# Optimization experiments

Hardware: AMD Instinct MI355X
Metric: run time of the kernel (lower is better)

The kernel has to match this reference:

```python
import jax, jax.numpy as jnp
import numpy as np

N = 12288      # number of nodes
D = 256        # in_features
K = 31         # k_neighbours + 1
EPS = 1e-12    # F.normalize eps


def setup_inputs() -> dict:
    key = jax.random.key(0)
    k1, k2, k3 = jax.random.split(key, 3)
    x = jax.random.normal(k1, (N, D), dtype=jnp.float32)
    # Attentive layer params: elementwise feature weights (torch init is ones;
    # perturb so the reference is non-degenerate)
    w0 = 1.0 + 0.1 * jax.random.normal(k2, (D,), dtype=jnp.float32)
    w1 = 1.0 + 0.1 * jax.random.normal(k3, (D,), dtype=jnp.float32)
    return {"x": x, "w0": w0, "w1": w1}


def reference(x, w0, w1):
    # internal_forward: relu(Attentive_0(x)) then Attentive_1 (last layer, no act)
    h = jax.nn.relu(x * w0)          # [N, D]
    h = h * w1                        # [N, D]
    # F.normalize(dim=-1, p=2)
    norm = jnp.sqrt(jnp.sum(h * h, axis=-1, keepdims=True))
    h = h / jnp.maximum(norm, EPS)
    # cal_similarity_graph: dense NxN similarity
    s = jnp.einsum('nd,md->nm', h, h)  # [N, N]
    # graph_top_K: keep top-K entries per row, zero the rest (scatter mask)
    _, idx = jax.lax.top_k(s, K)       # idx: [N, K]
    rows = jnp.arange(s.shape[0])[:, None]
    mask = jnp.zeros_like(s).at[rows, idx].set(1.0)
    # apply_non_linearity 'relu'
    return jax.nn.relu(s * mask)
```

## Files before the change

### kernel.cpp

```cpp
#include <hip/hip_runtime.h>
#include <cstdint>
#include <cstddef>
#include <math.h>

#define N_NODES 12288
#define D_FEAT  256
#define K_TOP   31

typedef float nfloat4 __attribute__((ext_vector_type(4)));

__device__ __forceinline__ float np_g(float xv, float w0v, float w1v) {
  #pragma clang fp contract(off)
  float t = __fmul_rn(xv, w0v);
  t = fmaxf(t, 0.0f);
  return __fmul_rn(t, w1v);
}

__device__ __forceinline__ void nt_store4(float* p, float4 v) {
  nfloat4 nv;
  nv.x = v.x; nv.y = v.y; nv.z = v.z; nv.w = v.w;
  __builtin_nontemporal_store(nv, reinterpret_cast<nfloat4*>(p));
}

__global__ __launch_bounds__(256) void np_norm_kernel(
    const float* __restrict__ x, const float* __restrict__ w0,
    const float* __restrict__ w1, float* __restrict__ nrm) {
  #pragma clang fp contract(off)
  const int n = blockIdx.x * blockDim.x + threadIdx.x;
  if (n >= N_NODES) return;
  const float* xr = x + (size_t)n * D_FEAT;
  float blk[2];
  #pragma unroll
  for (int b = 0; b < 2; ++b) {
    float r[8];
    #pragma unroll
    for (int j = 0; j < 8; ++j) {
      const int d = 128 * b + j;
      const float g = np_g(xr[d], w0[d], w1[d]);
      r[j] = __fmul_rn(g, g);
    }
    for (int i = 8; i < 128; i += 8) {
      #pragma unroll
      for (int j = 0; j < 8; ++j) {
        const int d = 128 * b + i + j;
        const float g = np_g(xr[d], w0[d], w1[d]);
        r[j] = __fadd_rn(r[j], __fmul_rn(g, g));
      }
    }
    blk[b] = __fadd_rn(
        __fadd_rn(__fadd_rn(r[0], r[1]), __fadd_rn(r[2], r[3])),
        __fadd_rn(__fadd_rn(r[4], r[5]), __fadd_rn(r[6], r[7])));
  }
  const float tot = __fadd_rn(blk[0], blk[1]);
  nrm[n] = fmaxf(__fsqrt_rn(tot), 1e-12f);
}

__global__ __launch_bounds__(256) void np_h_kernel(
    const float* __restrict__ x, const float* __restrict__ w0,
    const float* __restrict__ w1, const float* __restrict__ nrm,
    float* __restrict__ h) {
  #pragma clang fp contract(off)
  const int q = blockIdx.x * blockDim.x + threadIdx.x;
  const int base = q * 4;
  if (base >= N_NODES * D_FEAT) return;
  const int n = base >> 8;
  const int d = base & (D_FEAT - 1);
  const float ia = nrm[n];
  const float4 xv = *reinterpret_cast<const float4*>(&x[base]);
  const float4 w0v = *reinterpret_cast<const float4*>(&w0[d]);
  const float4 w1v = *reinterpret_cast<const float4*>(&w1[d]);
  float4 o;
  o.x = __fdiv_rn(np_g(xv.x, w0v.x, w1v.x), ia);
  o.y = __fdiv_rn(np_g(xv.y, w0v.y, w1v.y), ia);
  o.z = __fdiv_rn(np_g(xv.z, w0v.z, w1v.z), ia);
  o.w = __fdiv_rn(np_g(xv.w, w0v.w, w1v.w), ia);
  *reinterpret_cast<float4*>(&h[base]) = o;
}

#define BT 128
#define BK 32
#define TBW 132
#define NTILES (N_NODES / BT)
#define NBLOCKS (NTILES * (NTILES + 1) / 2)

template <int PRE>
__global__ __launch_bounds__(256, 4) void np_gemm_kernel(
    const float* __restrict__ x, const float* __restrict__ w0,
    const float* __restrict__ w1, const float* __restrict__ nrm,
    const float* __restrict__ h, float* __restrict__ out) {
  #pragma clang fp contract(off)
  __shared__ __align__(16) float smem[2 * BK * BT];
  float (*As)[BT] = reinterpret_cast<float (*)[BT]>(smem);
  float (*Bs)[BT] = reinterpret_cast<float (*)[BT]>(smem + BK * BT);
  float (*tb)[TBW] = reinterpret_cast<float (*)[TBW]>(smem);

  const int L = blockIdx.x;
  int by = (int)(96.5 - sqrt(96.5 * 96.5 - 2.0 * (double)L));
  while (by > 0 && by * NTILES - by * (by - 1) / 2 > L) --by;
  while ((by + 1) * NTILES - (by + 1) * by / 2 <= L) ++by;
  const int bx = by + (L - (by * NTILES - by * (by - 1) / 2));

  const int n0 = by * BT;
  const int m0 = bx * BT;
  const int t = threadIdx.x;
  const int tx = t & 15, ty = t >> 4;
  const int sr = t >> 1;
  const int sk = (t & 1) * 16;

  float acc[8][8] = {};

  for (int k0 = 0; k0 < D_FEAT; k0 += BK) {
    __syncthreads();
    if (PRE) {
      #pragma unroll
      for (int q = 0; q < 4; ++q) {
        const int c = sk + q * 4;
        const float4 ha = *reinterpret_cast<const float4*>(
            &h[(size_t)(n0 + sr) * D_FEAT + k0 + c]);
        const float4 hb = *reinterpret_cast<const float4*>(
            &h[(size_t)(m0 + sr) * D_FEAT + k0 + c]);
        As[c + 0][sr] = ha.x; As[c + 1][sr] = ha.y;
        As[c + 2][sr] = ha.z; As[c + 3][sr] = ha.w;
        Bs[c + 0][sr] = hb.x; Bs[c + 1][sr] = hb.y;
        Bs[c + 2][sr] = hb.z; Bs[c + 3][sr] = hb.w;
      }
    } else {
      const float ia = nrm[n0 + sr];
      const float ib = nrm[m0 + sr];
      #pragma unroll
      for (int q = 0; q < 4; ++q) {
        const int c = sk + q * 4;
        const float4 xa = *reinterpret_cast<const float4*>(
            &x[(size_t)(n0 + sr) * D_FEAT + k0 + c]);
        const float4 xb = *reinterpret_cast<const float4*>(
            &x[(size_t)(m0 + sr) * D_FEAT + k0 + c]);
        const float4 wa = *reinterpret_cast<const float4*>(&w0[k0 + c]);
        const float4 wb = *reinterpret_cast<const float4*>(&w1[k0 + c]);
        const float xaf[4] = {xa.x, xa.y, xa.z, xa.w};
        const float xbf[4] = {xb.x, xb.y, xb.z, xb.w};
        const float w0f[4] = {wa.x, wa.y, wa.z, wa.w};
        const float w1f[4] = {wb.x, wb.y, wb.z, wb.w};
        #pragma unroll
        for (int e = 0; e < 4; ++e) {
          As[c + e][sr] = __fdiv_rn(np_g(xaf[e], w0f[e], w1f[e]), ia);
          Bs[c + e][sr] = __fdiv_rn(np_g(xbf[e], w0f[e], w1f[e]), ib);
        }
      }
    }
    __syncthreads();

    for (int kk = 0; kk < BK; ++kk) {
      const float4 a0 = *reinterpret_cast<const float4*>(&As[kk][ty * 4]);
      const float4 a1 = *reinterpret_cast<const float4*>(&As[kk][64 + ty * 4]);
      const float4 b0 = *reinterpret_cast<const float4*>(&Bs[kk][tx * 4]);
      const float4 b1 = *reinterpret_cast<const float4*>(&Bs[kk][64 + tx * 4]);
      const float af[8] = {a0.x, a0.y, a0.z, a0.w, a1.x, a1.y, a1.z, a1.w};
      const float bf[8] = {b0.x, b0.y, b0.z, b0.w, b1.x, b1.y, b1.z, b1.w};
      #pragma unroll
      for (int i = 0; i < 8; ++i)
        #pragma unroll
        for (int j = 0; j < 8; ++j)
          acc[i][j] = __builtin_fmaf(af[i], bf[j], acc[i][j]);
    }
  }

  #pragma unroll
  for (int i = 0; i < 8; ++i) {
    const int row = n0 + (i >> 2) * 64 + ty * 4 + (i & 3);
    float4 o0, o1;
    o0.x = acc[i][0]; o0.y = acc[i][1]; o0.z = acc[i][2]; o0.w = acc[i][3];
    o1.x = acc[i][4]; o1.y = acc[i][5]; o1.z = acc[i][6]; o1.w = acc[i][7];
    nt_store4(&out[(size_t)row * N_NODES + m0 + tx * 4], o0);
    nt_store4(&out[(size_t)row * N_NODES + m0 + 64 + tx * 4], o1);
  }

  if (bx != by) {
    #pragma unroll
    for (int hh = 0; hh < 2; ++hh) {
      #pragma unroll
      for (int ss = 0; ss < 2; ++ss) {
        __syncthreads();
        if ((tx >> 3) == ss) {
          #pragma unroll
          for (int r = 0; r < 4; ++r) {
            const int j = hh * 4 + r;
            const int ml = (tx & 7) * 4 + r;
            #pragma unroll
            for (int ih = 0; ih < 2; ++ih) {
              float4 v;
              v.x = acc[ih * 4 + 0][j];
              v.y = acc[ih * 4 + 1][j];
              v.z = acc[ih * 4 + 2][j];
              v.w = acc[ih * 4 + 3][j];
              *reinterpret_cast<float4*>(&tb[ml][ih * 64 + ty * 4]) = v;
            }
          }
        }
        __syncthreads();
        #pragma unroll
        for (int p = 0; p < 4; ++p) {
          const int row = (t >> 5) + 8 * p;
          const int col = (t & 31) * 4;
          const float4 v = *reinterpret_cast<const float4*>(&tb[row][col]);
          nt_store4(
              &out[(size_t)(m0 + hh * 64 + ss * 32 + row) * N_NODES + n0 + col],
              v);
        }
      }
    }
  }
}

__device__ inline float att_decode(unsigned uu) {
  return (uu & 0x80000000u) ? __uint_as_float(uu & 0x7FFFFFFFu)
                            : __uint_as_float(~uu);
}

#define HBINS 2048

__global__ __launch_bounds__(256) void att_topk_kernel(float* __restrict__ s) {
  const int n = blockIdx.x;
  float* row = s + (size_t)n * N_NODES;
  const int t = threadIdx.x;
  const int lane = t & 63, wid = t >> 6;

  unsigned u[48];
#pragma unroll
  for (int i = 0; i < 12; ++i) {
    float4 v = reinterpret_cast<const float4*>(row)[t + 256 * i];
    const float f[4] = {v.x, v.y, v.z, v.w};
#pragma unroll
    for (int j = 0; j < 4; ++j) {
      unsigned b = __float_as_uint(f[j]);
      u[i * 4 + j] = (b & 0x80000000u) ? ~b : (b | 0x80000000u);
    }
  }

  __shared__ unsigned hist[HBINS];
  __shared__ unsigned wmn[4], wmx[4];
  __shared__ int wred[4];
  __shared__ unsigned bc_mn, bc_mx, bc_T;
  __shared__ int bc_B, bc_above, bc_cnt, bc_cand;
  __shared__ int cnt_s;

  unsigned mymn = u[0], mymx = u[0];
#pragma unroll
  for (int i = 1; i < 48; ++i) {
    mymn = u[i] < mymn ? u[i] : mymn;
    mymx = u[i] > mymx ? u[i] : mymx;
  }
#pragma unroll
  for (int o = 32; o > 0; o >>= 1) {
    const unsigned a = __shfl_down(mymn, o);
    const unsigned b = __shfl_down(mymx, o);
    mymn = a < mymn ? a : mymn;
    mymx = b > mymx ? b : mymx;
  }
  if (lane == 0) { wmn[wid] = mymn; wmx[wid] = mymx; }
  __syncthreads();
  if (t == 0) {
    unsigned mn = wmn[0], mx = wmx[0];
    for (int w = 1; w < 4; ++w) {
      mn = wmn[w] < mn ? wmn[w] : mn;
      mx = wmx[w] > mx ? wmx[w] : mx;
    }
    bc_mn = mn; bc_mx = mx;
  }
  __syncthreads();

  unsigned T;
  if (bc_mn == bc_mx) {
    T = bc_mn;
  } else {
    unsigned cur_lo = bc_mn;
    unsigned cur_range = bc_mx - bc_mn;
    int above_total = 0;
    bool done = false;
    for (int pass = 0; pass < 4 && !done; ++pass) {
      const int bits = 32 - __clz(cur_range);
      const int sh = bits > 11 ? bits - 11 : 0;
#pragma unroll
      for (int q = 0; q < HBINS / 256; ++q) hist[t + 256 * q] = 0u;
      __syncthreads();
#pragma unroll
      for (int i = 0; i < 48; ++i) {
        const unsigned rel = u[i] - cur_lo;
        if (u[i] >= cur_lo && rel <= cur_range)
          atomicAdd(&hist[rel >> sh], 1u);
      }
      __syncthreads();
      int hloc[8];
      int part = 0;
#pragma unroll
      for (int q = 0; q < 8; ++q) { hloc[q] = (int)hist[8 * t + q]; part += hloc[q]; }
      int v = part;
#pragma unroll
      for (int o = 1; o < 64; o <<= 1) {
        const int z = __shfl_down(v, o);
        if (lane + o < 64) v += z;
      }
      if (lane == 0) wred[wid] = v;
      __syncthreads();
      int wsuf = 0;
      for (int w = wid + 1; w < 4; ++w) wsuf += wred[w];
      const int suffix_incl = v + wsuf;
      int run = suffix_incl - part;
      int fB = -1, fAbove = 0, fCnt = 0;
#pragma unroll
      for (int q = 7; q >= 0; --q) {
        const int above = run;
        const int cnt = hloc[q];
        if (cnt > 0 && above_total + above < K_TOP &&
            above_total + above + cnt >= K_TOP) {
          fB = 8 * t + q; fAbove = above; fCnt = cnt;
        }
        run += cnt;
      }
      if (fB >= 0) { bc_B = fB; bc_above = fAbove; bc_cnt = fCnt; }
      __syncthreads();
      const int B = bc_B;
      const int aboveB = bc_above;
      const int cntB = bc_cnt;
      const unsigned bin_lo = cur_lo + ((unsigned)B << sh);
      if (sh == 0) {
        T = bin_lo;
        done = true;
      } else if (cntB <= HBINS) {
        if (t == 0) bc_cand = 0;
        __syncthreads();
#pragma unroll
        for (int i = 0; i < 48; ++i) {
          const unsigned rel = u[i] - cur_lo;
          if (u[i] >= cur_lo && rel <= cur_range && (int)(rel >> sh) == B) {
            const int slot = atomicAdd(&bc_cand, 1);
            hist[slot] = u[i];
          }
        }
        __syncthreads();
        const int m = bc_cand;
        const int kb = K_TOP - above_total - aboveB;
        for (int e = t; e < m; e += 256) {
          const unsigned ce = hist[e];
          int gt = 0, eq = 0;
          for (int e2 = 0; e2 < m; ++e2) {
            const unsigned c2 = hist[e2];
            gt += (c2 > ce) ? 1 : 0;
            eq += (c2 == ce) ? 1 : 0;
          }
          if (gt < kb && gt + eq >= kb) bc_T = ce;
        }
        __syncthreads();
        T = bc_T;
        done = true;
      } else {
        above_total += aboveB;
        cur_lo = bin_lo;
        cur_range = (1u << sh) - 1u;
      }
      __syncthreads();
    }
  }

  {
    int cg = 0, ce = 0;
#pragma unroll
    for (int i = 0; i < 48; ++i) {
      cg += (u[i] > T) ? 1 : 0;
      ce += (u[i] == T) ? 1 : 0;
    }
    int packed = (cg << 16) | ce;
#pragma unroll
    for (int o = 32; o > 0; o >>= 1) packed += __shfl_down(packed, o);
    if (t == 0) cnt_s = 0;
    __syncthreads();
    if ((t & 63) == 0) atomicAdd(&cnt_s, packed);
    __syncthreads();
  }
  const int tot = cnt_s;
  __syncthreads();
  const int tot_gt = tot >> 16;
  const int tot_eq = tot & 0xFFFF;
  const int need = K_TOP - tot_gt;

  if (tot_eq == need) {
#pragma unroll
    for (int i = 0; i < 12; ++i) {
      float vals[4];
#pragma unroll
      for (int j = 0; j < 4; ++j) {
        const unsigned uu = u[i * 4 + j];
        const float f = att_decode(uu);
        vals[j] = (uu >= T) ? fmaxf(f, 0.0f) : 0.0f;
      }
      float4 o; o.x = vals[0]; o.y = vals[1]; o.z = vals[2]; o.w = vals[3];
      reinterpret_cast<float4*>(row)[t + 256 * i] = o;
    }
  } else {
    __shared__ int eqc[12][256];
#pragma unroll
    for (int i = 0; i < 12; ++i) {
      int c = 0;
#pragma unroll
      for (int j = 0; j < 4; ++j) c += (u[i * 4 + j] == T) ? 1 : 0;
      eqc[i][t] = c;
    }
    __syncthreads();
    int base[12];
    {
      int run = 0;
      for (int i = 0; i < 12; ++i) {
        int pre = 0, tt_tot = 0;
        for (int tt = 0; tt < 256; ++tt) {
          const int vv = eqc[i][tt];
          if (tt < t) pre += vv;
          tt_tot += vv;
        }
        base[i] = run + pre;
        run += tt_tot;
      }
    }
#pragma unroll
    for (int i = 0; i < 12; ++i) {
      float vals[4];
      int r = base[i];
#pragma unroll
      for (int j = 0; j < 4; ++j) {
        const unsigned uu = u[i * 4 + j];
        const float f = att_decode(uu);
        bool keep = false;
        if (uu > T) keep = true;
        else if (uu == T) { keep = (r < need); ++r; }
        vals[j] = keep ? fmaxf(f, 0.0f) : 0.0f;
      }
      float4 o; o.x = vals[0]; o.y = vals[1]; o.z = vals[2]; o.w = vals[3];
      reinterpret_cast<float4*>(row)[t + 256 * i] = o;
    }
  }
}

extern "C" void kernel_launch(void* const* d_in, const int* in_sizes, int n_in,
                              void* d_out, int out_size, void* d_ws, size_t ws_size,
                              hipStream_t stream) {
  const float* x  = (const float*)d_in[0];
  const float* w0 = (const float*)d_in[1];
  const float* w1 = (const float*)d_in[2];
  float* out = (float*)d_out;
  float* nrm = (float*)d_ws;
  float* h = (float*)((char*)d_ws + 65536);

  const size_t need = 65536 + (size_t)N_NODES * D_FEAT * 4;

  np_norm_kernel<<<N_NODES / 256, 256, 0, stream>>>(x, w0, w1, nrm);

  if (ws_size >= need) {
    np_h_kernel<<<(N_NODES * D_FEAT / 4 + 255) / 256, 256, 0, stream>>>(
        x, w0, w1, nrm, h);
    np_gemm_kernel<1><<<NBLOCKS, 256, 0, stream>>>(x, w0, w1, nrm, h, out);
  } else {
    np_gemm_kernel<0><<<NBLOCKS, 256, 0, stream>>>(x, w0, w1, nrm, nullptr, out);
  }

  att_topk_kernel<<<N_NODES, 256, 0, stream>>>(out);
}
```

Measured before the change: 703.5 us.

## Use 128x256 paired-tile symmetric GEMM with 512 threads for precomputed path

Replaces the 128x128 triangular-tile GEMM on the precomputed-h path with a kernel that computes 128x256 tiles (two column tiles at once) using 512 threads. It writes both the direct and the transposed (mirrored) outputs, skipping the redundant lower-triangle tile. The aim is fewer blocks, more reuse of each A tile, and fewer launches' worth of scheduling overhead. The cost is more LDS and registers per block, some wasted compute on diagonal pairs, and a more complex block-to-tile mapping.

```diff
diff --git a/kernel.cpp b/kernel.cpp
--- a/kernel.cpp
+++ b/kernel.cpp
@@ -77,17 +77,133 @@
   *reinterpret_cast<float4*>(&h[base]) = o;
 }
 
-#define BT 128
 #define BK 32
 #define TBW 132
-#define NTILES (N_NODES / BT)
+#define NTILES 96
+#define NPBLOCKS 2352
+
+__global__ __launch_bounds__(512, 2) void np_gemm_pair_kernel(
+    const float* __restrict__ h, float* __restrict__ out) {
+  #pragma clang fp contract(off)
+  __shared__ __align__(16) float smem[BK * 128 + BK * 256];
+  float (*As)[128] = reinterpret_cast<float (*)[128]>(smem);
+  float (*Bs)[256] = reinterpret_cast<float (*)[256]>(smem + BK * 128);
+  float (*tb)[TBW] = reinterpret_cast<float (*)[TBW]>(smem);
+
+  const int L = blockIdx.x;
+  int by = 0, cum = 0;
+  while (cum + (48 - (by >> 1)) <= L) { cum += 48 - (by >> 1); ++by; }
+  const int p = (by >> 1) + (L - cum);
+
+  const int n0 = by * 128;
+  const int m0 = p * 256;
+  const int c0 = 2 * p;
+  const int c1 = 2 * p + 1;
+
+  const int t = threadIdx.x;
+  const int tx = t & 31, ty = t >> 5;
+
+  float acc[8][8] = {};
+
+  const int asr = t & 127;
+  const int ask = (t >> 7) * 8;
+  const int bsr = t & 255;
+  const int bsk = (t >> 8) * 16;
+
+  for (int k0 = 0; k0 < D_FEAT; k0 += BK) {
+    __syncthreads();
+    {
+      const float* ha = &h[(size_t)(n0 + asr) * D_FEAT + k0 + ask];
+      #pragma unroll
+      for (int q = 0; q < 2; ++q) {
+        const float4 v = *reinterpret_cast<const float4*>(&ha[q * 4]);
+        const int c = ask + q * 4;
+        As[c + 0][asr] = v.x; As[c + 1][asr] = v.y;
+        As[c + 2][asr] = v.z; As[c + 3][asr] = v.w;
+      }
+      const float* hb = &h[(size_t)(m0 + bsr) * D_FEAT + k0 + bsk];
+      #pragma unroll
+      for (int q = 0; q < 4; ++q) {
+        const float4 v = *reinterpret_cast<const float4*>(&hb[q * 4]);
+        const int c = bsk + q * 4;
+        Bs[c + 0][bsr] = v.x; Bs[c + 1][bsr] = v.y;
+        Bs[c + 2][bsr] = v.z; Bs[c + 3][bsr] = v.w;
+      }
+    }
+    __syncthreads();
+
+    for (int kk = 0; kk < BK; ++kk) {
+      const float4 a0 = *reinterpret_cast<const float4*>(&As[kk][ty * 4]);
+      const float4 a1 = *reinterpret_cast<const float4*>(&As[kk][64 + ty * 4]);
+      const float4 b0 = *reinterpret_cast<const float4*>(&Bs[kk][tx * 4]);
+      const float4 b1 = *reinterpret_cast<const float4*>(&Bs[kk][128 + tx * 4]);
+      const float af[8] = {a0.x, a0.y, a0.z, a0.w, a1.x, a1.y, a1.z, a1.w};
+      const float bf[8] = {b0.x, b0.y, b0.z, b0.w, b1.x, b1.y, b1.z, b1.w};
+      #pragma unroll
+      for (int i = 0; i < 8; ++i)
+        #pragma unroll
+        for (int j = 0; j < 8; ++j)
+          acc[i][j] = __builtin_fmaf(af[i], bf[j], acc[i][j]);
+    }
+  }
+
+  const bool store0 = (c0 >= by);
+  #pragma unroll
+  for (int i = 0; i < 8; ++i) {
+    const int row = n0 + (i >> 2) * 64 + ty * 4 + (i & 3);
+    if (store0) {
+      float4 o0;
+      o0.x = acc[i][0]; o0.y = acc[i][1]; o0.z = acc[i][2]; o0.w = acc[i][3];
+      nt_store4(&out[(size_t)row * N_NODES + m0 + tx * 4], o0);
+    }
+    float4 o1;
+    o1.x = acc[i][4]; o1.y = acc[i][5]; o1.z = acc[i][6]; o1.w = acc[i][7];
+    nt_store4(&out[(size_t)row * N_NODES + m0 + 128 + tx * 4], o1);
+  }
+
+  #pragma unroll
+  for (int q = 0; q < 2; ++q) {
+    const int c = 2 * p + q;
+    if (c <= by) continue;
+    #pragma unroll
+    for (int cc = 0; cc < 2; ++cc) {
+      __syncthreads();
+      if ((tx >> 4) == cc) {
+        #pragma unroll
+        for (int jj = 0; jj < 4; ++jj) {
+          const int mlr = (tx & 15) * 4 + jj;
+          #pragma unroll
+          for (int ih = 0; ih < 2; ++ih) {
+            float4 v;
+            v.x = acc[ih * 4 + 0][q * 4 + jj];
+            v.y = acc[ih * 4 + 1][q * 4 + jj];
+            v.z = acc[ih * 4 + 2][q * 4 + jj];
+            v.w = acc[ih * 4 + 3][q * 4 + jj];
+            *reinterpret_cast<float4*>(&tb[mlr][ih * 64 + ty * 4]) = v;
+          }
+        }
+      }
+      __syncthreads();
+      #pragma unroll
+      for (int qq = 0; qq < 4; ++qq) {
+        const int fid = t + 512 * qq;
+        const int row = fid >> 5;
+        const int colf = (fid & 31) * 4;
+        const float4 v = *reinterpret_cast<const float4*>(&tb[row][colf]);
+        nt_store4(
+            &out[(size_t)(c * 128 + cc * 64 + row) * N_NODES + n0 + colf], v);
+      }
+    }
+  }
+}
+
+#define BT 128
 #define NBLOCKS (NTILES * (NTILES + 1) / 2)
 
-template <int PRE>
 __global__ __launch_bounds__(256, 4) void np_gemm_kernel(
     const float* __restrict__ x, const float* __restrict__ w0,
     const float* __restrict__ w1, const float* __restrict__ nrm,
-    const float* __restrict__ h, float* __restrict__ out) {
+    float* __restrict__ out) {
   #pragma clang fp contract(off)
   __shared__ __align__(16) float smem[2 * BK * BT];
   float (*As)[BT] = reinterpret_cast<float (*)[BT]>(smem);
@@ -111,20 +227,7 @@
 
   for (int k0 = 0; k0 < D_FEAT; k0 += BK) {
     __syncthreads();
-    if (PRE) {
-      #pragma unroll
-      for (int q = 0; q < 4; ++q) {
-        const int c = sk + q * 4;
-        const float4 ha = *reinterpret_cast<const float4*>(
-            &h[(size_t)(n0 + sr) * D_FEAT + k0 + c]);
-        const float4 hb = *reinterpret_cast<const float4*>(
-            &h[(size_t)(m0 + sr) * D_FEAT + k0 + c]);
-        As[c + 0][sr] = ha.x; As[c + 1][sr] = ha.y;
-        As[c + 2][sr] = ha.z; As[c + 3][sr] = ha.w;
-        Bs[c + 0][sr] = hb.x; Bs[c + 1][sr] = hb.y;
-        Bs[c + 2][sr] = hb.z; Bs[c + 3][sr] = hb.w;
-      }
-    } else {
+    {
       const float ia = nrm[n0 + sr];
       const float ib = nrm[m0 + sr];
       #pragma unroll
@@ -148,7 +251,6 @@
       }
     }
     __syncthreads();
-
     for (int kk = 0; kk < BK; ++kk) {
       const float4 a0 = *reinterpret_cast<const float4*>(&As[kk][ty * 4]);
       const float4 a1 = *reinterpret_cast<const float4*>(&As[kk][64 + ty * 4]);
@@ -198,8 +300,8 @@
         }
         __syncthreads();
         #pragma unroll
-        for (int p = 0; p < 4; ++p) {
-          const int row = (t >> 5) + 8 * p;
+        for (int pq = 0; pq < 4; ++pq) {
+          const int row = (t >> 5) + 8 * pq;
           const int col = (t & 31) * 4;
           const float4 v = *reinterpret_cast<const float4*>(&tb[row][col]);
           nt_store4(
@@ -455,9 +557,9 @@
   if (ws_size >= need) {
     np_h_kernel<<<(N_NODES * D_FEAT / 4 + 255) / 256, 256, 0, stream>>>(
         x, w0, w1, nrm, h);
-    np_gemm_kernel<1><<<NBLOCKS, 256, 0, stream>>>(x, w0, w1, nrm, h, out);
+    np_gemm_pair_kernel<<<NPBLOCKS, 512, 0, stream>>>(h, out);
   } else {
-    np_gemm_kernel<0><<<NBLOCKS, 256, 0, stream>>>(x, w0, w1, nrm, nullptr, out);
+    np_gemm_kernel<<<NBLOCKS, 256, 0, stream>>>(x, w0, w1, nrm, out);
   }
 
   att_topk_kernel<<<N_NODES, 256, 0, stream>>>(out);
```

New measurement: 751.3 us. 6.8% more time.
